# Kernel optimization log

Hardware: AMD Instinct MI355X
Metric: run time of the kernel (lower is better)

Reference implementation:

```python
import jax, jax.numpy as jnp
import numpy as np

B, S, D = 2, 2048, 1024
H = 16
HD = D // H  # 64

def setup_inputs() -> dict:
    key = jax.random.key(0)
    ks = jax.random.split(key, 5)
    scale = 0.02
    x = jax.random.normal(ks[0], (B, S, D), dtype=jnp.float32)
    w_attn = jax.random.normal(ks[1], (D, 3 * D), dtype=jnp.float32) * scale
    b_attn = jnp.zeros((3 * D,), dtype=jnp.float32)
    w_proj = jax.random.normal(ks[2], (D, D), dtype=jnp.float32) * scale
    b_proj = jnp.zeros((D,), dtype=jnp.float32)
    return {"x": x, "w_attn": w_attn, "b_attn": b_attn, "w_proj": w_proj, "b_proj": b_proj}

def reference(x, w_attn, b_attn, w_proj, b_proj):
    b, s, d = x.shape
    qkv = x @ w_attn + b_attn                      # [B,S,3D]
    q, k, v = jnp.split(qkv, 3, axis=-1)
    # [B,H,S,HD]
    q = q.reshape(b, s, H, HD).transpose(0, 2, 1, 3)
    k = k.reshape(b, s, H, HD).transpose(0, 2, 1, 3)
    v = v.reshape(b, s, H, HD).transpose(0, 2, 1, 3)
    scores = jnp.einsum('bhqd,bhkd->bhqk', q, k) * (1.0 / np.sqrt(HD))
    causal = jnp.tril(jnp.ones((s, s), dtype=bool))
    scores = jnp.where(causal[None, None], scores, -jnp.inf)
    attn = jax.nn.softmax(scores, axis=-1)
    out = jnp.einsum('bhqk,bhkd->bhqd', attn, v)   # [B,H,S,HD]
    out = out.transpose(0, 2, 1, 3).reshape(b, s, d)
    return out @ w_proj + b_proj
```

## Files before the change

### kernel.cpp

```cpp
#include <hip/hip_runtime.h>

#define B_  2
#define S_  2048
#define D_  1024
#define H_  16
#define HD_ 64
#define TD_ 3072
#define M_  (B_*S_)
#define NWORK_ 24

using bf16x8 = __attribute__((ext_vector_type(8))) short;
using bf16x4 = __attribute__((ext_vector_type(4))) short;
using f32x4  = __attribute__((ext_vector_type(4))) float;

typedef __attribute__((address_space(1))) unsigned int uint_g;
typedef __attribute__((address_space(3))) unsigned int uint_l;

#define MFMA32 __builtin_amdgcn_mfma_f32_16x16x32_bf16

#if defined(__has_builtin)
#if __has_builtin(__builtin_amdgcn_mfma_f32_16x16x16_bf16_1k)
#define MFMA16(a,b,c) __builtin_amdgcn_mfma_f32_16x16x16_bf16_1k(a,b,c,0,0,0)
#define HAVE_MFMA16 1
#elif __has_builtin(__builtin_amdgcn_mfma_f32_16x16x16bf16_1k)
#define MFMA16(a,b,c) __builtin_amdgcn_mfma_f32_16x16x16bf16_1k(a,b,c,0,0,0)
#define HAVE_MFMA16 1
#endif
#endif
#ifndef HAVE_MFMA16
static __device__ __forceinline__ f32x4 MFMA16_stub(bf16x4 a, bf16x4 b, f32x4 c) { return c; }
#define MFMA16(a,b,c) MFMA16_stub(a,b,c)
#endif

static __device__ __forceinline__ short f2bf(float f) {
    unsigned u = __float_as_uint(f);
    u += 0x7FFFu + ((u >> 16) & 1u);
    return (short)(u >> 16);
}
static __device__ __forceinline__ unsigned pack2bf(float a, float b) {
    return (unsigned)(unsigned short)f2bf(a) | ((unsigned)(unsigned short)f2bf(b) << 16);
}
static __device__ __forceinline__ void gload_lds16(const short* g, short* l) {
    __builtin_amdgcn_global_load_lds((const uint_g*)g, (uint_l*)l, 16, 0, 0);
}
static __device__ __forceinline__ void unpack8(uint4 u, float* f) {
    unsigned a0 = u.x, a1 = u.y, a2 = u.z, a3 = u.w;
    f[0] = __uint_as_float(a0 << 16); f[1] = __uint_as_float(a0 & 0xFFFF0000u);
    f[2] = __uint_as_float(a1 << 16); f[3] = __uint_as_float(a1 & 0xFFFF0000u);
    f[4] = __uint_as_float(a2 << 16); f[5] = __uint_as_float(a2 & 0xFFFF0000u);
    f[6] = __uint_as_float(a3 << 16); f[7] = __uint_as_float(a3 & 0xFFFF0000u);
}

__global__ void cast_x_kernel(const float* __restrict__ x, short* __restrict__ xb, int n4) {
    int i = blockIdx.x * blockDim.x + threadIdx.x;
    if (i >= n4) return;
    float4 v = *((const float4*)x + i);
    short4 o;
    o.x = f2bf(v.x); o.y = f2bf(v.y); o.z = f2bf(v.z); o.w = f2bf(v.w);
    *((short4*)xb + i) = o;
}

__global__ __launch_bounds__(256)
void wtrans_kernel(const float* __restrict__ W, short* __restrict__ Wt, int K, int N) {
    __shared__ float T[32][33];
    int n0 = blockIdx.x * 32, k0 = blockIdx.y * 32;
    int tx = threadIdx.x & 31, ty = threadIdx.x >> 5;
    #pragma unroll
    for (int i = 0; i < 4; ++i)
        T[ty + i * 8][tx] = W[(size_t)(k0 + ty + i * 8) * N + n0 + tx];
    __syncthreads();
    #pragma unroll
    for (int i = 0; i < 4; ++i)
        Wt[(size_t)(n0 + ty + i * 8) * K + k0 + tx] = f2bf(T[tx][ty + i * 8]);
}

__global__ __launch_bounds__(256)
void vtrans_kernel(const short* __restrict__ V, short* __restrict__ Vt) {
    __shared__ short T[32][33];
    int p  = blockIdx.z;
    int s0 = blockIdx.x * 32;
    int d0 = blockIdx.y * 32;
    int tx = threadIdx.x & 31, ty = threadIdx.x >> 5;
    const short* Vp  = V  + (size_t)p * S_ * HD_;
    short*       Vtp = Vt + (size_t)p * HD_ * S_;
    #pragma unroll
    for (int i = 0; i < 4; ++i)
        T[ty + i * 8][tx] = Vp[(s0 + ty + i * 8) * HD_ + d0 + tx];
    __syncthreads();
    #pragma unroll
    for (int i = 0; i < 4; ++i)
        Vtp[(size_t)(d0 + ty + i * 8) * S_ + s0 + tx] = T[tx][ty + i * 8];
}

template<int MODE>
__global__ __launch_bounds__(256)
void gemm_mfma_kernel(const short* __restrict__ A, const short* __restrict__ Bt,
                      const float* __restrict__ bias, float* __restrict__ Cf,
                      short* __restrict__ Qo, short* __restrict__ Ko, short* __restrict__ Vo,
                      int M, int N, int K) {
    __shared__ __align__(16) short As[128 * 32];
    __shared__ __align__(16) short Bs[128 * 32];

    const int tid  = threadIdx.x;
    const int w    = tid >> 6, lane = tid & 63;
    const int quad = lane >> 4, l16 = lane & 15;
    const int wr = (w >> 1) * 64, wc = (w & 1) * 64;
    const int rowBase = blockIdx.y * 128, colBase = blockIdx.x * 128;

    f32x4 acc[4][4];
    const f32x4 zero = {0.f, 0.f, 0.f, 0.f};
    #pragma unroll
    for (int i = 0; i < 4; ++i)
        #pragma unroll
        for (int j = 0; j < 4; ++j) acc[i][j] = zero;

    const int srow = lane >> 2;
    const int scol = (lane & 3) * 8;

    for (int k0 = 0; k0 < K; k0 += 32) {
        __syncthreads();
        gload_lds16(A  + (size_t)(rowBase + w * 16 + srow)      * K + k0 + scol, &As[(w * 16) * 32]);
        gload_lds16(A  + (size_t)(rowBase + 64 + w * 16 + srow) * K + k0 + scol, &As[(64 + w * 16) * 32]);
        gload_lds16(Bt + (size_t)(colBase + w * 16 + srow)      * K + k0 + scol, &Bs[(w * 16) * 32]);
        gload_lds16(Bt + (size_t)(colBase + 64 + w * 16 + srow) * K + k0 + scol, &Bs[(64 + w * 16) * 32]);
        __syncthreads();

        bf16x8 af[4], bf[4];
        #pragma unroll
        for (int t = 0; t < 4; ++t) {
            af[t] = *(const bf16x8*)&As[(wr + t * 16 + l16) * 32 + quad * 8];
            bf[t] = *(const bf16x8*)&Bs[(wc + t * 16 + l16) * 32 + quad * 8];
        }
        #pragma unroll
        for (int i = 0; i < 4; ++i)
            #pragma unroll
            for (int j = 0; j < 4; ++j)
                acc[i][j] = MFMA32(af[i], bf[j], acc[i][j], 0, 0, 0);
    }

    if (MODE == 0) {
        #pragma unroll
        for (int i = 0; i < 4; ++i) {
            int row = rowBase + wr + i * 16 + quad * 4;
            #pragma unroll
            for (int j = 0; j < 4; ++j) {
                int col = colBase + wc + j * 16 + l16;
                float bv = bias[col];
                #pragma unroll
                for (int r = 0; r < 4; ++r)
                    Cf[(size_t)(row + r) * N + col] = acc[i][j][r] + bv;
            }
        }
    } else {
        #pragma unroll
        for (int j = 0; j < 4; ++j) {
            int col = colBase + wc + j * 16 + l16;
            int sel = col >> 10, cr = col & 1023;
            int h = cr >> 6, d = cr & 63;
            float bv  = bias[col];
            short* dst = (sel == 0) ? Qo : (sel == 1) ? Ko : Vo;
            float  scl = (sel == 0) ? 0.125f * 1.44269504f : 1.0f;
            #pragma unroll
            for (int i = 0; i < 4; ++i) {
                int row = rowBase + wr + i * 16 + quad * 4;
                #pragma unroll
                for (int r = 0; r < 4; ++r) {
                    int rw = row + r;
                    int bb = rw >> 11, s = rw & 2047;
                    dst[((size_t)(bb * H_ + h) * S_ + s) * HD_ + d] =
                        f2bf((acc[i][j][r] + bv) * scl);
                }
            }
        }
    }
}

__global__ __launch_bounds__(256, 3)
void flash_mfma_kernel(const short* __restrict__ Qg, const short* __restrict__ Kg,
                       const short* __restrict__ Vtg,
                       short* __restrict__ pO, float* __restrict__ pl) {
    __shared__ __align__(16) short Ks[64][72];
    __shared__ __align__(16) short Vs[64][72];

    const int plane_id = blockIdx.x;
    const int y = blockIdx.y;
    int qi, kc;
    if (y < 8) { qi = y; kc = 0; }
    else       { qi = 8 + ((y - 8) >> 1); kc = (y - 8) & 1; }
    int nkt = 2 * qi + 2 - kc * 16;
    if (nkt > 16) nkt = 16;
    const int kvOrigin = kc * 1024;

    const int tid  = threadIdx.x;
    const int w    = tid >> 6, lane = tid & 63;
    const int quad = lane >> 4, l16 = lane & 15;
    const int qBase = qi * 128;
    const size_t plane = (size_t)plane_id * S_ * HD_;

    const int sr0 = tid >> 3;
    const int sc0 = (tid & 7) * 8;

    const int qsubA = qBase + w * 32;
    const short* QrowA = Qg + plane + (size_t)(qsubA + l16) * HD_ + quad * 8;
    const bf16x8 qa0 = *(const bf16x8*)(QrowA);
    const bf16x8 qa1 = *(const bf16x8*)(QrowA + 32);
    const short* QrowB = QrowA + 16 * HD_;
    const bf16x8 qb0 = *(const bf16x8*)(QrowB);
    const bf16x8 qb1 = *(const bf16x8*)(QrowB + 32);

    f32x4 oA[4], oB[4];
    const f32x4 zero = {0.f, 0.f, 0.f, 0.f};
    #pragma unroll
    for (int i = 0; i < 4; ++i) { oA[i] = zero; oB[i] = zero; }
    float lA = 0.f, lB = 0.f;
    const int q_globA = qsubA + l16;
    const int q_globB = qsubA + 16 + l16;
    const int q_wave_max = qsubA + 31;

    uint4 ka0, ka1, va0, va1;
    ka0 = *(const uint4*)(Kg  + plane + (size_t)(kvOrigin + sr0)      * HD_ + sc0);
    ka1 = *(const uint4*)(Kg  + plane + (size_t)(kvOrigin + sr0 + 32) * HD_ + sc0);
    va0 = *(const uint4*)(Vtg + plane + (size_t)sr0        * S_ + kvOrigin + sc0);
    va1 = *(const uint4*)(Vtg + plane + (size_t)(sr0 + 32) * S_ + kvOrigin + sc0);

    for (int j = 0; j < nkt; ++j) {
        __syncthreads();
        *(uint4*)&Ks[sr0][sc0]      = ka0;
        *(uint4*)&Ks[sr0 + 32][sc0] = ka1;
        *(uint4*)&Vs[sr0][sc0]      = va0;
        *(uint4*)&Vs[sr0 + 32][sc0] = va1;
        __syncthreads();

        if (j + 1 < nkt) {
            const int kvB = kvOrigin + (j + 1) * 64;
            ka0 = *(const uint4*)(Kg  + plane + (size_t)(kvB + sr0)      * HD_ + sc0);
            ka1 = *(const uint4*)(Kg  + plane + (size_t)(kvB + sr0 + 32) * HD_ + sc0);
            va0 = *(const uint4*)(Vtg + plane + (size_t)sr0        * S_ + kvB + sc0);
            va1 = *(const uint4*)(Vtg + plane + (size_t)(sr0 + 32) * S_ + kvB + sc0);
        }

        const int kvBase = kvOrigin + j * 64;
        if (kvBase > q_wave_max) continue;

        f32x4 sA[4], sB[4];
        __builtin_amdgcn_s_setprio(1);
        #pragma unroll
        for (int ct = 0; ct < 4; ++ct) {
            bf16x8 kf0 = *(const bf16x8*)&Ks[ct * 16 + l16][quad * 8];
            bf16x8 kf1 = *(const bf16x8*)&Ks[ct * 16 + l16][32 + quad * 8];
            f32x4 a = zero, b = zero;
            a = MFMA32(kf0, qa0, a, 0, 0, 0);
            a = MFMA32(kf1, qa1, a, 0, 0, 0);
            b = MFMA32(kf0, qb0, b, 0, 0, 0);
            b = MFMA32(kf1, qb1, b, 0, 0, 0);
            sA[ct] = a; sB[ct] = b;
        }
        __builtin_amdgcn_s_setprio(0);

        if (kvBase + 63 > qsubA) {
            #pragma unroll
            for (int ct = 0; ct < 4; ++ct) {
                int kv = kvBase + ct * 16 + quad * 4;
                #pragma unroll
                for (int r = 0; r < 4; ++r)
                    if (kv + r > q_globA) sA[ct][r] = -3.0e38f;
            }
        }
        if (kvBase + 63 > qsubA + 16) {
            #pragma unroll
            for (int ct = 0; ct < 4; ++ct) {
                int kv = kvBase + ct * 16 + quad * 4;
                #pragma unroll
                for (int r = 0; r < 4; ++r)
                    if (kv + r > q_globB) sB[ct][r] = -3.0e38f;
            }
        }

        #pragma unroll
        for (int ct = 0; ct < 4; ++ct) {
            float pa0 = __builtin_amdgcn_exp2f(sA[ct][0]), pa1 = __builtin_amdgcn_exp2f(sA[ct][1]);
            float pa2 = __builtin_amdgcn_exp2f(sA[ct][2]), pa3 = __builtin_amdgcn_exp2f(sA[ct][3]);
            float pb0 = __builtin_amdgcn_exp2f(sB[ct][0]), pb1 = __builtin_amdgcn_exp2f(sB[ct][1]);
            float pb2 = __builtin_amdgcn_exp2f(sB[ct][2]), pb3 = __builtin_amdgcn_exp2f(sB[ct][3]);
            lA += (pa0 + pa1) + (pa2 + pa3);
            lB += (pb0 + pb1) + (pb2 + pb3);
            bf16x4 pA, pB;
            *(unsigned*)&pA       = pack2bf(pa0, pa1);
            *((unsigned*)&pA + 1) = pack2bf(pa2, pa3);
            *(unsigned*)&pB       = pack2bf(pb0, pb1);
            *((unsigned*)&pB + 1) = pack2bf(pb2, pb3);
            __builtin_amdgcn_s_setprio(1);
            #pragma unroll
            for (int dt = 0; dt < 4; ++dt) {
                bf16x4 vfr = *(const bf16x4*)&Vs[dt * 16 + l16][ct * 16 + quad * 4];
                oA[dt] = MFMA16(vfr, pA, oA[dt]);
                oB[dt] = MFMA16(vfr, pB, oB[dt]);
            }
            __builtin_amdgcn_s_setprio(0);
        }
    }

    lA += __shfl_xor(lA, 16); lA += __shfl_xor(lA, 32);
    lB += __shfl_xor(lB, 16); lB += __shfl_xor(lB, 32);
    const size_t lbase = ((size_t)plane_id * NWORK_ + y) * 128 + w * 32;
    if (quad == 0) {
        pl[lbase + l16]      = lA;
        pl[lbase + 16 + l16] = lB;
    }

    __syncthreads();
    short* Pw = (w < 2) ? &Ks[w * 32][0] : &Vs[(w - 2) * 32][0];
    #pragma unroll
    for (int dt = 0; dt < 4; ++dt) {
        uint2 ua, ub;
        ua.x = pack2bf(oA[dt][0], oA[dt][1]);
        ua.y = pack2bf(oA[dt][2], oA[dt][3]);
        ub.x = pack2bf(oB[dt][0], oB[dt][1]);
        ub.y = pack2bf(oB[dt][2], oB[dt][3]);
        *(uint2*)&Pw[l16 * 72 + dt * 16 + quad * 4]        = ua;
        *(uint2*)&Pw[(16 + l16) * 72 + dt * 16 + quad * 4] = ub;
    }
    __builtin_amdgcn_s_waitcnt(0xC07F);
    short* outBase = pO + (((size_t)plane_id * NWORK_ + y) * 128 + w * 32) * 64;
    #pragma unroll
    for (int pass = 0; pass < 4; ++pass) {
        int r  = pass * 8 + (lane >> 3);
        int cs = (lane & 7) * 8;
        uint4 vv = *(const uint4*)&Pw[r * 72 + cs];
        *(uint4*)(outBase + r * 64 + cs) = vv;
    }
}

__global__ __launch_bounds__(256)
void reduce_kernel(const short* __restrict__ pO, const float* __restrict__ pl,
                   short* __restrict__ atb) {
    const int plane_id = blockIdx.x, qi = blockIdx.y;
    const int h = plane_id & (H_ - 1), b = plane_id >> 4;
    const int tid = threadIdx.x;
    const int row = tid >> 1;
    const int cb  = (tid & 1) * 32;

    int t0, nch;
    if (qi < 8) { t0 = qi; nch = 1; }
    else        { t0 = 8 + 2 * (qi - 8); nch = 2; }

    const size_t pbase = (((size_t)plane_id * NWORK_ + t0) * 128 + row) * 64 + cb;
    float f[32], g[8];
    unpack8(*(const uint4*)(pO + pbase),      f);
    unpack8(*(const uint4*)(pO + pbase + 8),  f + 8);
    unpack8(*(const uint4*)(pO + pbase + 16), f + 16);
    unpack8(*(const uint4*)(pO + pbase + 24), f + 24);
    float l = pl[((size_t)plane_id * NWORK_ + t0) * 128 + row];
    if (nch == 2) {
        #pragma unroll
        for (int c = 0; c < 4; ++c) {
            unpack8(*(const uint4*)(pO + pbase + 8192 + c * 8), g);
            #pragma unroll
            for (int i = 0; i < 8; ++i) f[c * 8 + i] += g[i];
        }
        l += pl[((size_t)plane_id * NWORK_ + t0 + 1) * 128 + row];
    }
    const float inv = 1.0f / l;
    short* dst = atb + (size_t)(b * S_ + qi * 128 + row) * D_ + h * HD_ + cb;
    #pragma unroll
    for (int c = 0; c < 4; ++c) {
        uint2 o2;
        o2.x = pack2bf(f[c * 8 + 0] * inv, f[c * 8 + 1] * inv);
        o2.y = pack2bf(f[c * 8 + 2] * inv, f[c * 8 + 3] * inv);
        uint2 o3;
        o3.x = pack2bf(f[c * 8 + 4] * inv, f[c * 8 + 5] * inv);
        o3.y = pack2bf(f[c * 8 + 6] * inv, f[c * 8 + 7] * inv);
        uint4 ov; ov.x = o2.x; ov.y = o2.y; ov.z = o3.x; ov.w = o3.y;
        *(uint4*)(dst + c * 8) = ov;
    }
}

extern "C" void kernel_launch(void* const* d_in, const int* in_sizes, int n_in,
                              void* d_out, int out_size, void* d_ws, size_t ws_size,
                              hipStream_t stream) {
    const float* x      = (const float*)d_in[0];
    const float* w_attn = (const float*)d_in[1];
    const float* b_attn = (const float*)d_in[2];
    const float* w_proj = (const float*)d_in[3];
    const float* b_proj = (const float*)d_in[4];
    float* out = (float*)d_out;

    char* ws = (char*)d_ws;
    short* xb  = (short*)ws; ws += (size_t)M_ * D_ * 2;
    short* wat = (short*)ws; ws += (size_t)TD_ * D_ * 2;
    short* wpt = (short*)ws; ws += (size_t)D_ * D_ * 2;
    short* qg  = (short*)ws; ws += (size_t)M_ * D_ * 2;
    short* kg  = (short*)ws; ws += (size_t)M_ * D_ * 2;
    short* vg  = (short*)ws; ws += (size_t)M_ * D_ * 2;
    short* vtg = (short*)ws; ws += (size_t)M_ * D_ * 2;
    short* atb = (short*)ws; ws += (size_t)M_ * D_ * 2;

    short* pO = (short*)d_ws;
    float* pl = (float*)((char*)d_ws + (size_t)32 * NWORK_ * 128 * 64 * 2);

    cast_x_kernel<<<(M_ * D_ / 4 + 255) / 256, 256, 0, stream>>>(x, xb, M_ * D_ / 4);
    wtrans_kernel<<<dim3(TD_ / 32, D_ / 32), 256, 0, stream>>>(w_attn, wat, D_, TD_);
    wtrans_kernel<<<dim3(D_ / 32, D_ / 32), 256, 0, stream>>>(w_proj, wpt, D_, D_);

    gemm_mfma_kernel<1><<<dim3(TD_ / 128, M_ / 128), 256, 0, stream>>>(
        xb, wat, b_attn, nullptr, qg, kg, vg, M_, TD_, D_);

    vtrans_kernel<<<dim3(S_ / 32, HD_ / 32, B_ * H_), 256, 0, stream>>>(vg, vtg);

    flash_mfma_kernel<<<dim3(B_ * H_, NWORK_), 256, 0, stream>>>(qg, kg, vtg, pO, pl);

    reduce_kernel<<<dim3(B_ * H_, S_ / 128), 256, 0, stream>>>(pO, pl, atb);

    gemm_mfma_kernel<0><<<dim3(D_ / 128, M_ / 128), 256, 0, stream>>>(
        atb, wpt, b_proj, out, nullptr, nullptr, nullptr, M_, D_, D_);
}
```

Measured before the change: 197.7 us.

## Replace QKV GEMM with 256x256-tile direct-to-LDS pipelined MFMA kernel

```diff
diff --git a/kernel.cpp b/kernel.cpp
--- a/kernel.cpp
+++ b/kernel.cpp
@@ -92,6 +92,114 @@
         Vtp[(size_t)(d0 + ty + i * 8) * S_ + s0 + tx] = T[tx][ty + i * 8];
 }
 
+__global__ __launch_bounds__(512, 2)
+void gemm256_qkv_kernel(const short* __restrict__ A, const short* __restrict__ Bt,
+                        const float* __restrict__ bias,
+                        short* __restrict__ Qo, short* __restrict__ Ko, short* __restrict__ Vo,
+                        int M, int N, int K) {
+    __shared__ __align__(16) char lds[131072];
+
+    const int tid  = threadIdx.x;
+    const int w    = tid >> 6, lane = tid & 63;
+    const int quad = lane >> 4, l16 = lane & 15;
+    const int wm   = w >> 2,  wn  = w & 3;
+
+    const int gx  = gridDim.x;
+    const int nwg = gx * gridDim.y;
+    const int bid = blockIdx.y * gx + blockIdx.x;
+    const int sbid = (bid & 7) * (nwg >> 3) + (bid >> 3);
+    const int rowBase = (sbid / gx) * 256;
+    const int colBase = (sbid % gx) * 256;
+
+    const int scol = ((lane & 3) * 8) ^ ((lane & 32) >> 1);
+    const int sr0  = (w * 2) * 16 + (lane >> 2);
+    const short* Asrc0 = A  + (size_t)(rowBase + sr0)      * K + scol;
+    const short* Asrc1 = A  + (size_t)(rowBase + sr0 + 16) * K + scol;
+    const short* Bsrc0 = Bt + (size_t)(colBase + sr0)      * K + scol;
+    const short* Bsrc1 = Bt + (size_t)(colBase + sr0 + 16) * K + scol;
+
+    const int rterm = (l16 * 64 + quad * 16) ^ ((l16 & 8) << 2);
+    const char* ArdBase = lds + wm * 8192 + rterm;
+    const char* BrdBase = lds + 65536 + wn * 4096 + rterm;
+
+#define STAGE_A(t) { int sl_ = ((t) & 3) * 16384; \
+    gload_lds16(Asrc0 + (size_t)(t) * 32, (short*)(lds + sl_) + (w * 2)     * 512); \
+    gload_lds16(Asrc1 + (size_t)(t) * 32, (short*)(lds + sl_) + (w * 2 + 1) * 512); }
+#define STAGE_B(t) { int sl_ = 65536 + ((t) & 3) * 16384; \
+    gload_lds16(Bsrc0 + (size_t)(t) * 32, (short*)(lds + sl_) + (w * 2)     * 512); \
+    gload_lds16(Bsrc1 + (size_t)(t) * 32, (short*)(lds + sl_) + (w * 2 + 1) * 512); }
+
+    f32x4 acc[8][4];
+    const f32x4 zero = {0.f, 0.f, 0.f, 0.f};
+    #pragma unroll
+    for (int i = 0; i < 8; ++i)
+        #pragma unroll
+        for (int j = 0; j < 4; ++j) acc[i][j] = zero;
+
+    const int nk = K >> 5;
+    STAGE_A(0); STAGE_B(0);
+    STAGE_A(1); STAGE_B(1);
+
+    for (int t = 0; t < nk; ++t) {
+        if (t + 1 < nk) { asm volatile("s_waitcnt vmcnt(4)" ::: "memory"); }
+        else            { asm volatile("s_waitcnt vmcnt(0)" ::: "memory"); }
+        __builtin_amdgcn_s_barrier();
+        __builtin_amdgcn_sched_barrier(0);
+
+        const char* Ab = ArdBase + (t & 3) * 16384;
+        const char* Bb = BrdBase + (t & 3) * 16384;
+        bf16x8 bfr[4], afr[4];
+        #pragma unroll
+        for (int ni = 0; ni < 4; ++ni) bfr[ni] = *(const bf16x8*)(Bb + ni * 1024);
+        #pragma unroll
+        for (int mi = 0; mi < 4; ++mi) afr[mi] = *(const bf16x8*)(Ab + mi * 1024);
+        if (t + 2 < nk) STAGE_A(t + 2);
+
+        __builtin_amdgcn_s_setprio(1);
+        #pragma unroll
+        for (int mi = 0; mi < 4; ++mi)
+            #pragma unroll
+            for (int ni = 0; ni < 4; ++ni)
+                acc[mi][ni] = MFMA32(afr[mi], bfr[ni], acc[mi][ni], 0, 0, 0);
+        __builtin_amdgcn_s_setprio(0);
+
+        #pragma unroll
+        for (int mi = 0; mi < 4; ++mi) afr[mi] = *(const bf16x8*)(Ab + (4 + mi) * 1024);
+        if (t + 2 < nk) STAGE_B(t + 2);
+
+        __builtin_amdgcn_s_setprio(1);
+        #pragma unroll
+        for (int mi = 0; mi < 4; ++mi)
+            #pragma unroll
+            for (int ni = 0; ni < 4; ++ni)
+                acc[4 + mi][ni] = MFMA32(afr[mi], bfr[ni], acc[4 + mi][ni], 0, 0, 0);
+        __builtin_amdgcn_s_setprio(0);
+    }
+#undef STAGE_A
+#undef STAGE_B
+
+    #pragma unroll
+    for (int ni = 0; ni < 4; ++ni) {
+        int col = colBase + wn * 64 + ni * 16 + l16;
+        int sel = col >> 10, cr = col & 1023;
+        int h = cr >> 6, d = cr & 63;
+        float bv  = bias[col];
+        short* dst = (sel == 0) ? Qo : (sel == 1) ? Ko : Vo;
+        float  scl = (sel == 0) ? 0.125f * 1.44269504f : 1.0f;
+        #pragma unroll
+        for (int mi = 0; mi < 8; ++mi) {
+            int row = rowBase + wm * 128 + mi * 16 + quad * 4;
+            #pragma unroll
+            for (int r = 0; r < 4; ++r) {
+                int rw = row + r;
+                int bb = rw >> 11, s = rw & 2047;
+                dst[((size_t)(bb * H_ + h) * S_ + s) * HD_ + d] =
+                    f2bf((acc[mi][ni][r] + bv) * scl);
+            }
+        }
+    }
+}
+
 template<int MODE>
 __global__ __launch_bounds__(256)
 void gemm_mfma_kernel(const short* __restrict__ A, const short* __restrict__ Bt,
@@ -402,8 +510,8 @@
     wtrans_kernel<<<dim3(TD_ / 32, D_ / 32), 256, 0, stream>>>(w_attn, wat, D_, TD_);
     wtrans_kernel<<<dim3(D_ / 32, D_ / 32), 256, 0, stream>>>(w_proj, wpt, D_, D_);
 
-    gemm_mfma_kernel<1><<<dim3(TD_ / 128, M_ / 128), 256, 0, stream>>>(
-        xb, wat, b_attn, nullptr, qg, kg, vg, M_, TD_, D_);
+    gemm256_qkv_kernel<<<dim3(TD_ / 256, M_ / 256), 512, 0, stream>>>(
+        xb, wat, b_attn, qg, kg, vg, M_, TD_, D_);
 
     vtrans_kernel<<<dim3(S_ / 32, HD_ / 32, B_ * H_), 256, 0, stream>>>(vg, vtg);
 
```

After: 193.2 us. 2.2% less time.
